# Kernel optimization log

Hardware: AMD Instinct MI355X
Metric: run time of the kernel (lower is better)

Reference implementation:

```python
import jax, jax.numpy as jnp
import numpy as np
from functools import partial

DT = 1e-3
TAU_SYN_INV = 200.0  # norse default 1/5e-3
TAU_MEM_INV = 100.0  # norse default 1/1e-2

@partial(jax.custom_vjp, nondiff_argnums=(1,))
def superspike(x, alpha):
    return (x > 0).astype(x.dtype)

def _ss_fwd(x, alpha):
    return (x > 0).astype(x.dtype), x

def _ss_bwd(alpha, x, g):
    return (g / (alpha * jnp.abs(x) + 1.0) ** 2,)

superspike.defvjp(_ss_fwd, _ss_bwd)

def conv2d(x, w, b):
    y = jax.lax.conv_general_dilated(x, w, (1, 1), 'VALID',
                                     dimension_numbers=('NCHW', 'OIHW', 'NCHW'))
    return y + b[None, :, None, None]

def maxpool3(x):
    return jax.lax.reduce_window(x, -jnp.inf, jax.lax.max,
                                 (1, 1, 3, 3), (1, 1, 3, 3), 'VALID')

def lif_ff(inp, state, v_th, alpha):
    # norse feed-forward LIF: decay v and i, spike, reset, inject input current
    v, i = state
    v_dec = v + DT * TAU_MEM_INV * (-v + i)   # v_leak = 0
    i_dec = i - DT * TAU_SYN_INV * i
    z = superspike(v_dec - v_th, alpha)
    v_new = (1.0 - z) * v_dec                  # v_reset = 0
    return z, (v_new, i_dec + inp)

def lif_rec(inp, state, w_in, w_rec, v_th, alpha):
    # norse recurrent LIF: recurrent current uses PREVIOUS step's spikes
    z, v, i = state
    v_dec = v + DT * TAU_MEM_INV * (-v + i)
    i_dec = i - DT * TAU_SYN_INV * i
    z_new = superspike(v_dec - v_th, alpha)
    v_new = (1.0 - z_new) * v_dec
    i_new = i_dec + inp @ w_in.T + z @ w_rec.T
    return z_new, (z_new, v_new, i_new)

def li(inp, state):
    # leaky integrator readout (no spiking)
    v, i = state
    v_new = v + DT * TAU_MEM_INV * (-v + i)
    i_new = i - DT * TAU_SYN_INV * i + inp
    return v_new, (v_new, i_new)

def setup_inputs() -> dict:
    key = jax.random.key(0)
    ks = jax.random.split(key, 9)
    B, T, C, H, W = 32, 150, 2, 34, 34
    HID = 512
    x = jax.random.uniform(ks[0], (B, T, C, H, W), dtype=jnp.float32)
    def w(k, shape, fan_in):
        return jax.random.normal(k, shape, dtype=jnp.float32) / np.float32(np.sqrt(fan_in))
    return {
        'x': x,
        'conv1_w': w(ks[1], (30, 2, 7, 7), 2 * 49),
        'conv1_b': jnp.zeros((30,), jnp.float32),
        'conv2_w': w(ks[2], (70, 30, 5, 5), 30 * 25),
        'conv2_b': jnp.zeros((70,), jnp.float32),
        'l1_in_w': w(ks[3], (HID, 70), 70),
        'l1_rec_w': w(ks[4], (HID, HID), HID),
        'fc_out_w': w(ks[5], (4, HID), HID),
        'cl_in_w': w(ks[6], (2 * HID, 70), 70),
        'cl_rec_w': w(ks[7], (2 * HID, 2 * HID), 2 * HID),
        'cl_fc_w': w(ks[8], (10, 2 * HID), 2 * HID),
    }

def reference(x, conv1_w, conv1_b, conv2_w, conv2_b,
              l1_in_w, l1_rec_w, fc_out_w, cl_in_w, cl_rec_w, cl_fc_w):
    B = x.shape[0]
    HID = l1_in_w.shape[0]
    z0 = lambda *s: jnp.zeros(s, x.dtype)
    carry0 = (
        (z0(B, 30, 9, 9), z0(B, 30, 9, 9)),             # lif0 (v, i)
        (z0(B, 70, 1, 1), z0(B, 70, 1, 1)),             # lif1 (v, i)
        (z0(B, HID), z0(B, HID), z0(B, HID)),           # l1 (z, v, i)
        (z0(B, 4), z0(B, 4)),                            # out LI (v, i)
        (z0(B, 2 * HID), z0(B, 2 * HID), z0(B, 2 * HID)),# cl_l1 (z, v, i)
        (z0(B, 10), z0(B, 10)),                          # cl_out LI (v, i)
    )

    def step(carry, zt):
        s0, s2, s1, so, s1c, soc = carry
        z = maxpool3(conv2d(zt, conv1_w, conv1_b))       # (B,30,9,9)
        z, s0 = lif_ff(z, s0, 1.0, 100.0)
        z = maxpool3(conv2d(z, conv2_w, conv2_b))        # (B,70,1,1)
        z, s2 = lif_ff(z, s2, 1.0, 100.0)
        z = z.reshape(B, -1)                             # (B,70)
        z1, s1 = lif_rec(z, s1, l1_in_w, l1_rec_w, 0.4, 10.0)
        vo, so = li(z1 @ fc_out_w.T, so)
        z1c, s1c = lif_rec(z, s1c, cl_in_w, cl_rec_w, 0.4, 10.0)
        voc, soc = li(z1c @ cl_fc_w.T, soc)
        return (s0, s2, s1, so, s1c, soc), (vo, voc)

    _, (vos, vocs) = jax.lax.scan(step, carry0, jnp.swapaxes(x, 0, 1))
    y_hat = jnp.max(vos, axis=0)                         # (B,4)
    log_probs = jax.nn.log_softmax(jnp.max(vocs, axis=0), axis=1)  # (B,10)
    return y_hat, log_probs
```

## Files before the change

kernel.cpp:

```cpp
#include <hip/hip_runtime.h>
#include <math.h>


#define BATCH 32
#define TSTEPS 150
#define C1N 1470
#define ZSEQN 70
#define HID1 512
#define HID2 1024
#define K1CAT 582
#define K2CAT 1094

#define N_W1T  (K1CAT*HID1)
#define N_W2T  (K2CAT*HID2)

#define A1_U64  (BATCH*TSTEPS*32)
#define A0_U64  (BATCH*TSTEPS*16)
#define AC_U64  (BATCH*TSTEPS*8)
#define N_ARCH_U64 (A1_U64+A0_U64+AC_U64)

typedef unsigned long long u64;

__global__ void setup_misc(const float* __restrict__ l1_in_w,
                           const float* __restrict__ l1_rec_w,
                           const float* __restrict__ cl_in_w,
                           const float* __restrict__ cl_rec_w,
                           float* __restrict__ w1t,
                           float* __restrict__ w2t,
                           u64* __restrict__ arch) {
    int idx = blockIdx.x * blockDim.x + threadIdx.x;
    int stride = gridDim.x * blockDim.x;
    for (int e = idx; e < N_W1T; e += stride) {
        int j = e / HID1, o = e - j * HID1;
        w1t[e] = (j < HID1) ? l1_rec_w[o * HID1 + j] : l1_in_w[o * 70 + (j - HID1)];
    }
    for (int e = idx; e < N_W2T; e += stride) {
        int j = e / HID2, o = e - j * HID2;
        w2t[e] = (j < HID2) ? cl_rec_w[o * HID2 + j] : cl_in_w[o * 70 + (j - HID2)];
    }
    for (int e = idx; e < N_ARCH_U64; e += stride) arch[e] = 0ull;
}

__global__ __launch_bounds__(640) void conv1_pool(const float* __restrict__ x,
                                                  const float* __restrict__ w1,
                                                  const float* __restrict__ b1,
                                                  float* __restrict__ c1buf,
                                                  int b0) {
    __shared__ float img[2 * 34 * 34];
    __shared__ float w1s[30 * 2 * 49];
    __shared__ float crow[630 * 21];
    int tid = threadIdx.x;
    for (int e = tid; e < 2940; e += 640) w1s[e] = w1[e];
    #pragma unroll
    for (int k = 0; k < 2; ++k) {
        int f = blockIdx.x * 2 + k;
        int bl = f / TSTEPS, ts = f - bl * TSTEPS;
        const float* xin = x + ((size_t)(b0 + bl) * TSTEPS + ts) * 2312;
        __syncthreads();
        for (int e = tid; e < 2312; e += 640) img[e] = xin[e];
        __syncthreads();
        if (tid < 630) {
            int oc = tid / 21, cy = tid - oc * 21;
            float acc[21];
            #pragma unroll
            for (int j = 0; j < 21; ++j) acc[j] = 0.f;
            #pragma unroll
            for (int ic = 0; ic < 2; ++ic) {
                const float* irow0 = &img[ic * 1156];
                const float* wrow = &w1s[(oc * 2 + ic) * 49];
                #pragma unroll
                for (int ky = 0; ky < 7; ++ky) {
                    const float* ir = &irow0[(cy + ky) * 34];
                    float r[27];
                    #pragma unroll
                    for (int j = 0; j < 27; ++j) r[j] = ir[j];
                    #pragma unroll
                    for (int kx = 0; kx < 7; ++kx) {
                        float w = wrow[ky * 7 + kx];
                        #pragma unroll
                        for (int cx = 0; cx < 21; ++cx)
                            acc[cx] = fmaf(r[cx + kx], w, acc[cx]);
                    }
                }
            }
            #pragma unroll
            for (int cx = 0; cx < 21; ++cx) crow[tid * 21 + cx] = acc[cx];
        }
        __syncthreads();
        float* c1 = c1buf + (size_t)f * C1N;
        for (int p = tid; p < C1N; p += 640) {
            int oc = p / 49; int r = p - oc * 49; int py = r / 7, px = r - py * 7;
            float m = -1e30f;
            #pragma unroll
            for (int dy = 0; dy < 3; ++dy) {
                int rowid = oc * 21 + 3 * py + dy;
                #pragma unroll
                for (int dx = 0; dx < 3; ++dx)
                    m = fmaxf(m, crow[rowid * 21 + 3 * px + dx]);
            }
            c1[p] = m + b1[oc];
        }
    }
}

__device__ __forceinline__ float4 f4add(float4 a, const float4 b) {
    a.x += b.x; a.y += b.y; a.z += b.z; a.w += b.w; return a;
}
__device__ __forceinline__ void ast64(u64* p, u64 v) {
    __hip_atomic_store(p, v, __ATOMIC_RELAXED, __HIP_MEMORY_SCOPE_AGENT);
}
__device__ __forceinline__ u64 ald64(const u64* p) {
    return __hip_atomic_load((u64*)p, __ATOMIC_RELAXED, __HIP_MEMORY_SCOPE_AGENT);
}

__device__ __forceinline__ void conv_body(int w, int bl,
        const float* __restrict__ w2, const float* __restrict__ b2,
        const float* __restrict__ c1buf,
        u64* __restrict__ ac, float* smem) {
    const int ocStart2 = w * 9;
    const int nOc2 = (w == 7) ? 7 : 9;
    float* z0f  = smem;
    float* part = smem + 1472;
    float* red  = smem + 3904;

    const int t = threadIdx.x;
    float v0r[6], i0r[6], cf[6];
    #pragma unroll
    for (int k = 0; k < 6; ++k) { v0r[k] = 0.f; i0r[k] = 0.f; }
    float v2 = 0.f, i2 = 0.f;
    float bias2 = (t < nOc2) ? b2[ocStart2 + t] : 0.f;
    const float* c1 = c1buf + (size_t)bl * TSTEPS * C1N;
    #pragma unroll
    for (int k = 0; k < 6; ++k) {
        int e = t + k * 256;
        cf[k] = (e < C1N) ? c1[e] : 0.f;
    }
    if (t == 0) ast64(ac + w, ((u64)1 << 32));
    __syncthreads();

    for (int tt = 0; tt < TSTEPS; ++tt) {
        float nf[6];
        bool h = (tt + 1 < TSTEPS);
        if (h) {
            const float* c1n = c1 + (size_t)(tt + 1) * C1N;
            #pragma unroll
            for (int k = 0; k < 6; ++k) {
                int e = t + k * 256;
                nf[k] = (e < C1N) ? c1n[e] : 0.f;
            }
        }
        #pragma unroll
        for (int k = 0; k < 6; ++k) {
            int e = t + k * 256;
            if (e < C1N) {
                float vd = v0r[k] + 0.1f * (i0r[k] - v0r[k]);
                bool sp = (vd > 1.0f);
                v0r[k] = sp ? 0.f : vd;
                i0r[k] = i0r[k] - 0.2f * i0r[k] + cf[k];
                z0f[e] = sp ? 1.f : 0.f;
            }
        }
        __syncthreads();
        #pragma unroll
        for (int pass = 0; pass < 2; ++pass) {
            int u = t + pass * 256;
            if (u < nOc2 * 30) {
                int ol = u / 30, ic = u - ol * 30;
                float zw[49];
                #pragma unroll
                for (int j = 0; j < 49; ++j) zw[j] = z0f[ic * 49 + j];
                float a[9];
                #pragma unroll
                for (int p = 0; p < 9; ++p) a[p] = 0.f;
                const float* wb = w2 + (size_t)(ocStart2 + ol) * 750 + ic * 25;
                #pragma unroll
                for (int ky = 0; ky < 5; ++ky)
                    #pragma unroll
                    for (int kx = 0; kx < 5; ++kx) {
                        float wvv = wb[ky * 5 + kx];
                        #pragma unroll
                        for (int cy = 0; cy < 3; ++cy)
                            #pragma unroll
                            for (int cx = 0; cx < 3; ++cx)
                                a[cy * 3 + cx] = fmaf(zw[(cy + ky) * 7 + cx + kx], wvv, a[cy * 3 + cx]);
                    }
                #pragma unroll
                for (int p = 0; p < 9; ++p) part[u * 9 + p] = a[p];
            }
        }
        __syncthreads();
        if (t < nOc2 * 9) {
            int ol = t / 9, pos = t - ol * 9;
            float s2 = 0.f;
            for (int ic = 0; ic < 30; ++ic) s2 += part[(ol * 30 + ic) * 9 + pos];
            red[t] = s2;
        }
        __syncthreads();
        bool sp2 = false;
        if (t < nOc2) {
            float m = -1e30f;
            #pragma unroll
            for (int p = 0; p < 9; ++p) m = fmaxf(m, red[t * 9 + p]);
            float inp = m + bias2;
            float id2 = i2 - 0.2f * i2;
            i2 = id2 + inp;
            float vd2 = v2 + 0.1f * (i2 - v2);
            sp2 = (vd2 > 1.0f);
            v2 = sp2 ? 0.f : vd2;
        }
        if (tt + 1 < TSTEPS) {
            u64 mz2 = __ballot(sp2);
            if (t == 0)
                ast64(ac + (size_t)(tt + 1) * 8 + w,
                      (((u64)(tt + 2)) << 32) | (mz2 & 0x1ffull));
        }
        #pragma unroll
        for (int k = 0; k < 6; ++k) cf[k] = nf[k];
    }
}

template <int ROLE>
__device__ __forceinline__ void stripe_body(int b, int s,
        const float* __restrict__ catT,
        u64* __restrict__ arch,
        const u64* __restrict__ ac,
        float* smem) {
    constexpr int N    = ROLE ? HID2 : HID1;
    constexpr int K    = ROLE ? K2CAT : K1CAT;
    constexpr int SW   = N / 32;
    constexpr int NW   = N / 32;
    constexpr int NWT  = NW + 3;
    constexpr int N4   = N / 4;
    constexpr int COLS = ROLE ? 64 : 128;
    constexpr int QC   = COLS / 4;
    constexpr int S    = 256 / QC;
    constexpr int PSTR = COLS + 4;

    float* part = smem;
    unsigned short* list = (unsigned short*)(smem + 1088);
    unsigned int* maskw = (unsigned int*)(smem + 1088 + 547);
    unsigned int* wprefix = maskw + 40;

    const int t = threadIdx.x;
    const int lane = t & 63, wv = t >> 6;
    const int aid = t / QC, qid = t - (t / QC) * QC;
    const int q0 = s * QC;

    const float4* __restrict__ catT4 = (const float4*)catT;
    float v = 0.f, iacc = 0.f;

    if (wv == 0) {
        bool needc = (lane >= 40 && lane < 48);
        u64 cw = 0;
        for (;;) {
            if (needc) cw = ald64(ac + (lane - 40));
            bool ok = !needc || (unsigned)(cw >> 32) == 1u;
            if (__ballot(ok) == ~0ull) break;
            __builtin_amdgcn_s_sleep(1);
        }
        if (lane < NW) maskw[lane] = 0u;
        u64 lo = 0, hi = 0;
        #pragma unroll
        for (int w = 0; w < 8; ++w) {
            u64 p = (u64)(__shfl((unsigned)cw, 40 + w) & 0x1ffu);
            if (w < 7) lo |= p << (9 * w);
            else { lo |= (p & 1ull) << 63; hi = p >> 1; }
        }
        if (lane == 0) {
            maskw[NW] = (unsigned)lo; maskw[NW + 1] = (unsigned)(lo >> 32);
            maskw[NW + 2] = (unsigned)hi;
        }
        unsigned val = (lane < NWT) ? __popc(maskw[lane]) : 0u;
        #pragma unroll
        for (int d = 1; d < 64; d <<= 1) {
            unsigned u2 = __shfl_up(val, d);
            if (lane >= d) val += u2;
        }
        if (lane < NWT) wprefix[lane + 1] = val;
        if (lane == 0) wprefix[0] = 0u;
    }
    __syncthreads();
    int A = wprefix[NWT];
    for (int jj = t; jj < K; jj += 256) {
        unsigned m = maskw[jj >> 5];
        if ((m >> (jj & 31)) & 1u)
            list[wprefix[jj >> 5] + __popc(m & ((1u << (jj & 31)) - 1u))] = (unsigned short)jj;
    }
    __syncthreads();

    for (int tt = 0; tt < TSTEPS; ++tt) {
        float vd = v + 0.1f * (iacc - v);
        bool sp = (t < COLS) && (vd > 0.4f);
        float znew = sp ? 1.f : 0.f;
        if (t < COLS) v = sp ? 0.f : vd;
        u64 mz = __ballot(znew != 0.f);
        if (lane == 0 && wv < COLS / 64) {
            u64 tag = ((u64)(tt + 1)) << 32;
            u64* wslot = arch + (size_t)tt * SW + s * (COLS / 32) + wv * 2;
            ast64(wslot,     tag | (unsigned)(mz & 0xffffffffull));
            ast64(wslot + 1, tag | (unsigned)(mz >> 32));
        }
        float4 s0 = {0.f, 0.f, 0.f, 0.f}, s1 = s0, s2 = s0, s3 = s0;
        int idx = aid;
        for (; idx + 3 * S < A; idx += 4 * S) {
            s0 = f4add(s0, catT4[(size_t)list[idx]         * N4 + q0 + qid]);
            s1 = f4add(s1, catT4[(size_t)list[idx + S]     * N4 + q0 + qid]);
            s2 = f4add(s2, catT4[(size_t)list[idx + 2 * S] * N4 + q0 + qid]);
            s3 = f4add(s3, catT4[(size_t)list[idx + 3 * S] * N4 + q0 + qid]);
        }
        for (; idx < A; idx += S) s0 = f4add(s0, catT4[(size_t)list[idx] * N4 + q0 + qid]);
        s0 = f4add(f4add(s0, s1), f4add(s2, s3));
        *(float4*)(part + aid * PSTR + 4 * qid) = s0;
        __syncthreads();
        if (t < COLS) {
            float cur = 0.f;
            #pragma unroll
            for (int a = 0; a < S; ++a) cur += part[a * PSTR + t];
            iacc = iacc - 0.2f * iacc + cur;
        }
        if (tt + 1 >= TSTEPS) break;
        if (wv == 0) {
            bool needr = lane < SW;
            bool needc = (lane >= 40 && lane < 48);
            u64 wr = 0, wc = 0;
            for (;;) {
                if (needr) wr = ald64(arch + (size_t)tt * SW + lane);
                if (needc) wc = ald64(ac + (size_t)(tt + 1) * 8 + (lane - 40));
                bool ok = (!needr || (unsigned)(wr >> 32) == (unsigned)(tt + 1))
                       && (!needc || (unsigned)(wc >> 32) == (unsigned)(tt + 2));
                if (__ballot(ok) == ~0ull) break;
                __builtin_amdgcn_s_sleep(1);
            }
            if (needr) maskw[lane] = (unsigned)wr;
            u64 lo = 0, hi = 0;
            #pragma unroll
            for (int w = 0; w < 8; ++w) {
                u64 p = (u64)(__shfl((unsigned)wc, 40 + w) & 0x1ffu);
                if (w < 7) lo |= p << (9 * w);
                else { lo |= (p & 1ull) << 63; hi = p >> 1; }
            }
            if (lane == 0) {
                maskw[NW] = (unsigned)lo; maskw[NW + 1] = (unsigned)(lo >> 32);
                maskw[NW + 2] = (unsigned)hi;
            }
            unsigned val = (lane < NWT) ? __popc(maskw[lane]) : 0u;
            #pragma unroll
            for (int d = 1; d < 64; d <<= 1) {
                unsigned u2 = __shfl_up(val, d);
                if (lane >= d) val += u2;
            }
            if (lane < NWT) wprefix[lane + 1] = val;
            if (lane == 0) wprefix[0] = 0u;
        }
        __syncthreads();
        A = wprefix[NWT];
        for (int jj = t; jj < K; jj += 256) {
            unsigned m = maskw[jj >> 5];
            if ((m >> (jj & 31)) & 1u)
                list[wprefix[jj >> 5] + __popc(m & ((1u << (jj & 31)) - 1u))] = (unsigned short)jj;
        }
        __syncthreads();
    }
}

template <int ROLE>
__device__ __forceinline__ void readout_body(int b,
        const float* __restrict__ fcw,
        const u64* __restrict__ arch,
        float* __restrict__ out, float* smem) {
    constexpr int N  = ROLE ? HID2 : HID1;
    constexpr int SW = N / 32;
    constexpr int R  = ROLE ? 10 : 4;

    unsigned int* zw = (unsigned int*)smem;
    float* wpart = smem + 32;
    float* mvals = smem + 72;

    const int t = threadIdx.x;
    const int lane = t & 63, wv = t >> 6;
    float vli = 0.f, ili = 0.f, rmax = -1e30f;

    for (int tt = 0; tt < TSTEPS; ++tt) {
        if (wv == 0) {
            bool need = lane < SW;
            u64 w = 0;
            for (;;) {
                if (need) w = ald64(arch + (size_t)tt * SW + lane);
                bool ok = !need || (unsigned)(w >> 32) == (unsigned)(tt + 1);
                if (__ballot(ok) == ~0ull) break;
                __builtin_amdgcn_s_sleep(1);
            }
            if (need) zw[lane] = (unsigned)w;
        }
        __syncthreads();
        #pragma unroll
        for (int k = 0; k < R; ++k) {
            float p;
            if (ROLE) {
                unsigned bits = (zw[(t * 4) >> 5] >> ((t * 4) & 31)) & 0xFu;
                float4 w4 = ((const float4*)fcw)[k * (N / 4) + t];
                p = (bits & 1u ? w4.x : 0.f) + (bits & 2u ? w4.y : 0.f)
                  + (bits & 4u ? w4.z : 0.f) + (bits & 8u ? w4.w : 0.f);
            } else {
                unsigned bits = (zw[(t * 2) >> 5] >> ((t * 2) & 31)) & 0x3u;
                float2 w2 = ((const float2*)fcw)[k * (N / 2) + t];
                p = (bits & 1u ? w2.x : 0.f) + (bits & 2u ? w2.y : 0.f);
            }
            #pragma unroll
            for (int off = 32; off; off >>= 1) p += __shfl_xor(p, off);
            if (lane == 0) wpart[k * 4 + wv] = p;
        }
        __syncthreads();
        if (t < R) {
            float inp = wpart[t * 4] + wpart[t * 4 + 1] + wpart[t * 4 + 2] + wpart[t * 4 + 3];
            float vn = vli + 0.1f * (ili - vli);
            ili = ili - 0.2f * ili + inp;
            vli = vn;
            rmax = fmaxf(rmax, vn);
        }
    }
    if (ROLE) {
        if (t < 10) mvals[t] = rmax;
        __syncthreads();
        if (t < 10) {
            float M = -1e30f;
            #pragma unroll
            for (int k = 0; k < 10; ++k) M = fmaxf(M, mvals[k]);
            float ssum = 0.f;
            #pragma unroll
            for (int k = 0; k < 10; ++k) ssum += expf(mvals[k] - M);
            out[BATCH * 4 + b * 10 + t] = mvals[t] - M - logf(ssum);
        }
    } else if (t < 4) {
        out[b * 4 + t] = rmax;
    }
}

__global__ __launch_bounds__(256, 4) void snn_fused(
        const float* __restrict__ w2, const float* __restrict__ b2,
        const float* __restrict__ fc_out_w, const float* __restrict__ cl_fc_w,
        const float* __restrict__ w1t, const float* __restrict__ w2t,
        const float* __restrict__ c1buf,
        u64* __restrict__ arch1, u64* __restrict__ arch0,
        u64* __restrict__ archc,
        float* __restrict__ out, int b0, int BP) {
    __shared__ float smem[4096];
    int bid = blockIdx.x;
    if (bid < 8 * BP) {
        int w = bid / BP, bl = bid - w * BP;
        int b = b0 + bl;
        conv_body(w, bl, w2, b2, c1buf,
                  archc + (size_t)b * TSTEPS * 8, smem);
    } else if (bid < 24 * BP) {
        int idx = bid - 8 * BP;
        int s = idx / BP, bl = idx - s * BP;
        int b = b0 + bl;
        stripe_body<1>(b, s, w2t, arch1 + (size_t)b * TSTEPS * 32,
                       archc + (size_t)b * TSTEPS * 8, smem);
    } else if (bid < 28 * BP) {
        int idx = bid - 24 * BP;
        int s = idx / BP, bl = idx - s * BP;
        int b = b0 + bl;
        stripe_body<0>(b, s, w1t, arch0 + (size_t)b * TSTEPS * 16,
                       archc + (size_t)b * TSTEPS * 8, smem);
    } else if (bid < 29 * BP) {
        int b = b0 + (bid - 28 * BP);
        readout_body<1>(b, cl_fc_w, arch1 + (size_t)b * TSTEPS * 32, out, smem);
    } else {
        int b = b0 + (bid - 29 * BP);
        readout_body<0>(b, fc_out_w, arch0 + (size_t)b * TSTEPS * 16, out, smem);
    }
}

extern "C" void kernel_launch(void* const* d_in, const int* in_sizes, int n_in,
                              void* d_out, int out_size, void* d_ws, size_t ws_size,
                              hipStream_t stream) {
    const float* x        = (const float*)d_in[0];
    const float* w1       = (const float*)d_in[1];
    const float* b1       = (const float*)d_in[2];
    const float* w2       = (const float*)d_in[3];
    const float* b2       = (const float*)d_in[4];
    const float* l1_in_w  = (const float*)d_in[5];
    const float* l1_rec_w = (const float*)d_in[6];
    const float* fc_out_w = (const float*)d_in[7];
    const float* cl_in_w  = (const float*)d_in[8];
    const float* cl_rec_w = (const float*)d_in[9];
    const float* cl_fc_w  = (const float*)d_in[10];
    float* out = (float*)d_out;

    u64* arch1  = (u64*)d_ws;
    u64* arch0  = arch1 + A1_U64;
    u64* archc  = arch0 + A0_U64;
    float* w1t  = (float*)(archc + AC_U64);
    float* w2t  = w1t + N_W1T;
    float* c1buf = w2t + N_W2T;

    size_t head = 2 * (size_t)N_ARCH_U64 + N_W1T + N_W2T;
    size_t avail = ws_size / 4;
    int BP = 4;
    if (head + (size_t)32 * TSTEPS * C1N <= avail) BP = 32;
    else if (head + (size_t)16 * TSTEPS * C1N <= avail) BP = 16;
    else if (head + (size_t)8 * TSTEPS * C1N <= avail) BP = 8;

    setup_misc<<<dim3(256), dim3(256), 0, stream>>>(l1_in_w, l1_rec_w,
                                                    cl_in_w, cl_rec_w,
                                                    w1t, w2t, arch1);
    for (int b0 = 0; b0 < BATCH; b0 += BP) {
        conv1_pool<<<dim3(BP * TSTEPS / 2), dim3(640), 0, stream>>>(x, w1, b1, c1buf, b0);
        snn_fused<<<dim3(30 * BP), dim3(256), 0, stream>>>(w2, b2, fc_out_w, cl_fc_w,
                                                           w1t, w2t, c1buf,
                                                           arch1, arch0, archc,
                                                           out, b0, BP);
    }
}
```

Baseline: 719.8 us.

## Prefetch spike-mask flags early, pad conv1 image rows, regroup stripe blocks by batch

After: 776.4 us. +7.9%, slower.

```diff
diff --git a/kernel.cpp b/kernel.cpp
--- a/kernel.cpp
+++ b/kernel.cpp
@@ -46,7 +46,7 @@
                                                   const float* __restrict__ b1,
                                                   float* __restrict__ c1buf,
                                                   int b0) {
-    __shared__ float img[2 * 34 * 34];
+    __shared__ float img[2 * 34 * 36];
     __shared__ float w1s[30 * 2 * 49];
     __shared__ float crow[630 * 21];
     int tid = threadIdx.x;
@@ -57,7 +57,11 @@
         int bl = f / TSTEPS, ts = f - bl * TSTEPS;
         const float* xin = x + ((size_t)(b0 + bl) * TSTEPS + ts) * 2312;
         __syncthreads();
-        for (int e = tid; e < 2312; e += 640) img[e] = xin[e];
+        for (int e = tid; e < 2312; e += 640) {
+            int ic = e / 1156, rr = e - ic * 1156;
+            int y = rr / 34, xx = rr - y * 34;
+            img[ic * 1224 + y * 36 + xx] = xin[e];
+        }
         __syncthreads();
         if (tid < 630) {
             int oc = tid / 21, cy = tid - oc * 21;
@@ -66,14 +70,15 @@
             for (int j = 0; j < 21; ++j) acc[j] = 0.f;
             #pragma unroll
             for (int ic = 0; ic < 2; ++ic) {
-                const float* irow0 = &img[ic * 1156];
+                const float* irow0 = &img[ic * 1224];
                 const float* wrow = &w1s[(oc * 2 + ic) * 49];
                 #pragma unroll
                 for (int ky = 0; ky < 7; ++ky) {
-                    const float* ir = &irow0[(cy + ky) * 34];
-                    float r[27];
+                    const float* ir = &irow0[(cy + ky) * 36];
+                    float r[28];
                     #pragma unroll
-                    for (int j = 0; j < 27; ++j) r[j] = ir[j];
+                    for (int j4 = 0; j4 < 7; ++j4)
+                        *(float4*)&r[4 * j4] = *(const float4*)&ir[4 * j4];
                     #pragma unroll
                     for (int kx = 0; kx < 7; ++kx) {
                         float w = wrow[ky * 7 + kx];
@@ -300,6 +305,13 @@
             ast64(wslot,     tag | (unsigned)(mz & 0xffffffffull));
             ast64(wslot + 1, tag | (unsigned)(mz >> 32));
         }
+        const bool needr = (wv == 0) && (lane < SW);
+        const bool needc = (wv == 0) && (lane >= 40 && lane < 48);
+        u64 wr = 0, wc = 0;
+        if (tt + 1 < TSTEPS) {
+            if (needr) wr = ald64(arch + (size_t)tt * SW + lane);
+            if (needc) wc = ald64(ac + (size_t)(tt + 1) * 8 + (lane - 40));
+        }
         float4 s0 = {0.f, 0.f, 0.f, 0.f}, s1 = s0, s2 = s0, s3 = s0;
         int idx = aid;
         for (; idx + 3 * S < A; idx += 4 * S) {
@@ -320,16 +332,15 @@
         }
         if (tt + 1 >= TSTEPS) break;
         if (wv == 0) {
-            bool needr = lane < SW;
-            bool needc = (lane >= 40 && lane < 48);
-            u64 wr = 0, wc = 0;
             for (;;) {
-                if (needr) wr = ald64(arch + (size_t)tt * SW + lane);
-                if (needc) wc = ald64(ac + (size_t)(tt + 1) * 8 + (lane - 40));
                 bool ok = (!needr || (unsigned)(wr >> 32) == (unsigned)(tt + 1))
                        && (!needc || (unsigned)(wc >> 32) == (unsigned)(tt + 2));
                 if (__ballot(ok) == ~0ull) break;
                 __builtin_amdgcn_s_sleep(1);
+                if (needr && (unsigned)(wr >> 32) != (unsigned)(tt + 1))
+                    wr = ald64(arch + (size_t)tt * SW + lane);
+                if (needc && (unsigned)(wc >> 32) != (unsigned)(tt + 2))
+                    wc = ald64(ac + (size_t)(tt + 1) * 8 + (lane - 40));
             }
             if (needr) maskw[lane] = (unsigned)wr;
             u64 lo = 0, hi = 0;
@@ -378,21 +389,25 @@
 
     const int t = threadIdx.x;
     const int lane = t & 63, wv = t >> 6;
+    const bool need = (wv == 0) && (lane < SW);
     float vli = 0.f, ili = 0.f, rmax = -1e30f;
 
+    u64 wpre = need ? ald64(arch + lane) : 0;
     for (int tt = 0; tt < TSTEPS; ++tt) {
         if (wv == 0) {
-            bool need = lane < SW;
-            u64 w = 0;
+            u64 w = wpre;
             for (;;) {
-                if (need) w = ald64(arch + (size_t)tt * SW + lane);
                 bool ok = !need || (unsigned)(w >> 32) == (unsigned)(tt + 1);
                 if (__ballot(ok) == ~0ull) break;
                 __builtin_amdgcn_s_sleep(1);
+                if (need && (unsigned)(w >> 32) != (unsigned)(tt + 1))
+                    w = ald64(arch + (size_t)tt * SW + lane);
             }
             if (need) zw[lane] = (unsigned)w;
         }
         __syncthreads();
+        if (need && tt + 1 < TSTEPS)
+            wpre = ald64(arch + (size_t)(tt + 1) * SW + lane);
         #pragma unroll
         for (int k = 0; k < R; ++k) {
             float p;
@@ -453,13 +468,13 @@
                   archc + (size_t)b * TSTEPS * 8, smem);
     } else if (bid < 24 * BP) {
         int idx = bid - 8 * BP;
-        int s = idx / BP, bl = idx - s * BP;
+        int bl = idx >> 4, s = idx & 15;
         int b = b0 + bl;
         stripe_body<1>(b, s, w2t, arch1 + (size_t)b * TSTEPS * 32,
                        archc + (size_t)b * TSTEPS * 8, smem);
     } else if (bid < 28 * BP) {
         int idx = bid - 24 * BP;
-        int s = idx / BP, bl = idx - s * BP;
+        int bl = idx >> 2, s = idx & 3;
         int b = b0 + bl;
         stripe_body<0>(b, s, w1t, arch0 + (size_t)b * TSTEPS * 16,
                        archc + (size_t)b * TSTEPS * 8, smem);
```
